# Optimization experiments

Measured on AMD Instinct MI355X. Metric: run time of the kernel, lower is better.

## Reference

```python
import jax, jax.numpy as jnp
import numpy as np

H = 256
VOCAB = 32000
B = 128
T = 2048


def setup_inputs() -> dict:
    key = jax.random.key(0)
    ks = jax.random.split(key, 14)
    s = 0.05
    return {
        "tokens": jax.random.randint(ks[0], (B, 1), 0, VOCAB),
        "hidden": jax.random.normal(ks[1], (1, B, H), jnp.float32),
        "encoder_outputs": jax.random.normal(ks[2], (T, B, H), jnp.float32),
        "emb_table": jax.random.normal(ks[3], (VOCAB + 1, H), jnp.float32) * s,
        "attn_W": jax.random.normal(ks[4], (1, 2 * H), jnp.float32) * s,
        "attn_b": jax.random.normal(ks[5], (1,), jnp.float32) * s,
        "comb_W": jax.random.normal(ks[6], (H, 2 * H), jnp.float32) * s,
        "comb_b": jax.random.normal(ks[7], (H,), jnp.float32) * s,
        "gru_Wih": jax.random.normal(ks[8], (3 * H, H), jnp.float32) * s,
        "gru_Whh": jax.random.normal(ks[9], (3 * H, H), jnp.float32) * s,
        "gru_bih": jax.random.normal(ks[10], (3 * H,), jnp.float32) * s,
        "gru_bhh": jax.random.normal(ks[11], (3 * H,), jnp.float32) * s,
        "out_W": jax.random.normal(ks[12], (VOCAB, H), jnp.float32) * s,
        "out_b": jax.random.normal(ks[13], (VOCAB,), jnp.float32) * s,
    }


def reference(tokens, hidden, encoder_outputs, emb_table, attn_W, attn_b,
              comb_W, comb_b, gru_Wih, gru_Whh, gru_bih, gru_bhh, out_W, out_b):
    h = hidden.shape[-1]
    # Embedding lookup: [B,1] -> [B,1,H] -> [1,B,H]
    emb = jnp.transpose(emb_table[tokens], (1, 0, 2))
    # Additive attention: Linear([hidden; enc_t]) -> scalar score per position.
    # attn_W splits into hidden part (first H cols) and encoder part (last H).
    W_h, W_e = attn_W[:, :h], attn_W[:, h:]          # [1,H] each
    scores = (jnp.einsum('tbh,oh->tbo', encoder_outputs, W_e)
              + jnp.einsum('lbh,oh->lbo', hidden, W_h)  # broadcast over T
              + attn_b)                                  # [T,B,1]
    attn_w = jax.nn.softmax(scores, axis=0)              # softmax over time
    # Context: weighted sum over time -> [1,B,H]
    ctx = jnp.einsum('tbo,tbh->obh', attn_w, encoder_outputs)
    # Combine embedded input with context, relu
    x = jnp.concatenate([emb, ctx], axis=2)              # [1,B,2H]
    x = jax.nn.relu(jnp.einsum('lbk,hk->lbh', x, comb_W) + comb_b)  # [1,B,H]
    # Single GRU step (PyTorch gate ordering: r, z, n)
    gx = x[0] @ gru_Wih.T + gru_bih                      # [B,3H]
    gh = hidden[0] @ gru_Whh.T + gru_bhh                 # [B,3H]
    r = jax.nn.sigmoid(gx[:, :h] + gh[:, :h])
    z = jax.nn.sigmoid(gx[:, h:2 * h] + gh[:, h:2 * h])
    n = jnp.tanh(gx[:, 2 * h:] + r * gh[:, 2 * h:])
    h_new = ((1.0 - z) * n + z * hidden[0])[None]        # [1,B,H]
    # Output projection + log_softmax over vocab
    logits = jnp.einsum('lbh,vh->lbv', h_new, out_W) + out_b
    logp = jax.nn.log_softmax(logits, axis=2)            # [1,B,V]
    return (logp, h_new, jnp.transpose(attn_w, (1, 0, 2)), ctx)
```

## Files before the change

kernel.cpp:

```cpp
#include <hip/hip_runtime.h>
#include <cstddef>

constexpr int H  = 256;
constexpr int Bb = 128;
constexpr int T  = 2048;
constexpr int V  = 32000;
constexpr int SPLITS = 16;
constexpr int TC = T / SPLITS;
constexpr int NPART = SPLITS * 4;
constexpr int NBLK = V / 64;

typedef __attribute__((ext_vector_type(8))) short short8;
typedef __attribute__((ext_vector_type(4))) float f32x4;

__device__ __forceinline__ unsigned short bf1(float a) {
  unsigned u = __builtin_bit_cast(unsigned, a);
  return (unsigned short)((u + 0x7fffu + ((u >> 16) & 1u)) >> 16);
}
__device__ __forceinline__ unsigned bfpack2(float a, float b) {
  unsigned ua = __builtin_bit_cast(unsigned, a);
  unsigned ub = __builtin_bit_cast(unsigned, b);
  ua = (ua + 0x7fffu + ((ua >> 16) & 1u)) >> 16;
  ub = (ub + 0x7fffu + ((ub >> 16) & 1u)) & 0xffff0000u;
  return ua | ub;
}

__global__ __launch_bounds__(256) void k_attn(
    const float* __restrict__ enc, const float* __restrict__ hidden,
    const float* __restrict__ attn_W, const float* __restrict__ attn_b,
    float* __restrict__ scores, float* __restrict__ ctx_part) {
  const int b = blockIdx.y, chunk = blockIdx.x;
  const int tid = threadIdx.x, lane = tid & 63, wave = tid >> 6;

  const float4 we = *(const float4*)(attn_W + H + lane * 4);
  const float4 wh = *(const float4*)(attn_W + lane * 4);
  const float4 hv = *(const float4*)(hidden + (size_t)b * H + lane * 4);

  float hb = fmaf(wh.x, hv.x, fmaf(wh.y, hv.y, fmaf(wh.z, hv.z, wh.w * hv.w)));
  #pragma unroll
  for (int off = 1; off < 64; off <<= 1) hb += __shfl_xor(hb, off);
  hb += attn_b[0];

  const int t0 = chunk * TC + wave * 32;
  const float* base = enc + (size_t)t0 * (Bb * H) + (size_t)b * H + lane * 4;

  float4 acc = {0.f, 0.f, 0.f, 0.f};
  for (int i = 0; i < 32; i += 4) {
    float4 e0 = *(const float4*)(base + (size_t)(i + 0) * (Bb * H));
    float4 e1 = *(const float4*)(base + (size_t)(i + 1) * (Bb * H));
    float4 e2 = *(const float4*)(base + (size_t)(i + 2) * (Bb * H));
    float4 e3 = *(const float4*)(base + (size_t)(i + 3) * (Bb * H));

    float p0 = fmaf(e0.x, we.x, fmaf(e0.y, we.y, fmaf(e0.z, we.z, e0.w * we.w)));
    float p1 = fmaf(e1.x, we.x, fmaf(e1.y, we.y, fmaf(e1.z, we.z, e1.w * we.w)));
    float p2 = fmaf(e2.x, we.x, fmaf(e2.y, we.y, fmaf(e2.z, we.z, e2.w * we.w)));
    float p3 = fmaf(e3.x, we.x, fmaf(e3.y, we.y, fmaf(e3.z, we.z, e3.w * we.w)));
    #pragma unroll
    for (int off = 1; off < 64; off <<= 1) {
      p0 += __shfl_xor(p0, off);
      p1 += __shfl_xor(p1, off);
      p2 += __shfl_xor(p2, off);
      p3 += __shfl_xor(p3, off);
    }
    float s0 = p0 + hb, s1 = p1 + hb, s2 = p2 + hb, s3 = p3 + hb;
    float w0 = __expf(s0), w1 = __expf(s1), w2 = __expf(s2), w3 = __expf(s3);

    acc.x = fmaf(w0, e0.x, fmaf(w1, e1.x, fmaf(w2, e2.x, fmaf(w3, e3.x, acc.x))));
    acc.y = fmaf(w0, e0.y, fmaf(w1, e1.y, fmaf(w2, e2.y, fmaf(w3, e3.y, acc.y))));
    acc.z = fmaf(w0, e0.z, fmaf(w1, e1.z, fmaf(w2, e2.z, fmaf(w3, e3.z, acc.z))));
    acc.w = fmaf(w0, e0.w, fmaf(w1, e1.w, fmaf(w2, e2.w, fmaf(w3, e3.w, acc.w))));

    if (lane == 0) {
      float4 sv = {s0, s1, s2, s3};
      *(float4*)(scores + (size_t)b * T + t0 + i) = sv;
    }
  }
  float* cp = ctx_part + ((size_t)b * NPART + chunk * 4 + wave) * H + lane * 4;
  *(float4*)cp = acc;
}

__global__ __launch_bounds__(256) void k_ctx_gru(
    const float* __restrict__ scores, const float* __restrict__ ctx_part,
    float* __restrict__ attn_o, float* __restrict__ ctx_o,
    const int* __restrict__ tokens, const float* __restrict__ hidden,
    const float* __restrict__ emb_table,
    const float* __restrict__ comb_W, const float* __restrict__ comb_b,
    const float* __restrict__ Wih, const float* __restrict__ Whh,
    const float* __restrict__ bih, const float* __restrict__ bhh,
    float* __restrict__ hnew, unsigned short* __restrict__ hnewb) {
  const int b = blockIdx.x, tid = threadIdx.x;
  const int lane = tid & 63, wave = tid >> 6;
  const int g4 = lane >> 2, l4 = lane & 3;
  __shared__ float red[4];
  __shared__ float m_sh, l_sh;
  __shared__ __align__(16) float x2[2 * H];
  __shared__ __align__(16) float hid[H];
  __shared__ __align__(16) float xs[H];
  __shared__ float Ar[H], Az[H], Cn[H], Dn[H];

  const float* sb = scores + (size_t)b * T;
  float s[8];
  #pragma unroll
  for (int q = 0; q < 8; q++) s[q] = sb[tid + 256 * q];

  float mx = s[0];
  #pragma unroll
  for (int q = 1; q < 8; q++) mx = fmaxf(mx, s[q]);
  #pragma unroll
  for (int off = 1; off < 64; off <<= 1) mx = fmaxf(mx, __shfl_xor(mx, off));
  if (lane == 0) red[wave] = mx;
  __syncthreads();
  if (tid == 0) m_sh = fmaxf(fmaxf(red[0], red[1]), fmaxf(red[2], red[3]));
  __syncthreads();
  const float m = m_sh;

  float w[8];
  float ps = 0.f;
  #pragma unroll
  for (int q = 0; q < 8; q++) { w[q] = __expf(s[q] - m); ps += w[q]; }
  #pragma unroll
  for (int off = 1; off < 64; off <<= 1) ps += __shfl_xor(ps, off);
  __syncthreads();
  if (lane == 0) red[wave] = ps;
  __syncthreads();
  if (tid == 0) l_sh = red[0] + red[1] + red[2] + red[3];
  __syncthreads();
  const float inv = 1.f / l_sh;

  #pragma unroll
  for (int q = 0; q < 8; q++) attn_o[(size_t)b * T + tid + 256 * q] = w[q] * inv;

  float c = 0.f;
  for (int si = 0; si < NPART; si++)
    c += ctx_part[((size_t)b * NPART + si) * H + tid];
  const float cval = c * __expf(-m) * inv;
  ctx_o[(size_t)b * H + tid] = cval;

  x2[tid]     = emb_table[(size_t)tokens[b] * H + tid];
  x2[H + tid] = cval;
  hid[tid]    = hidden[(size_t)b * H + tid];
  __syncthreads();

  #pragma unroll 1
  for (int batch = 0; batch < 4; batch++) {
    const int row = wave * 64 + batch * 16 + g4;
    const float* wr = comb_W + (size_t)row * (2 * H);
    float p = 0.f;
    #pragma unroll 8
    for (int i = 0; i < 32; i++) {
      const int o = i * 16 + l4 * 4;
      float4 wv = *(const float4*)(wr + o);
      float4 xv = *(const float4*)(x2 + o);
      p = fmaf(wv.x, xv.x, fmaf(wv.y, xv.y, fmaf(wv.z, xv.z, fmaf(wv.w, xv.w, p))));
    }
    p += __shfl_xor(p, 1);
    p += __shfl_xor(p, 2);
    if (l4 == 0) xs[row] = fmaxf(p + comb_b[row], 0.f);
  }
  __syncthreads();

  #pragma unroll 1
  for (int batch = 0; batch < 4; batch++) {
    const int row = wave * 64 + batch * 16 + g4;
    const float* wxr = Wih + (size_t)row * H;
    const float* wxz = Wih + (size_t)(row + H) * H;
    const float* wxn = Wih + (size_t)(row + 2 * H) * H;
    const float* whr = Whh + (size_t)row * H;
    const float* whz = Whh + (size_t)(row + H) * H;
    const float* whn = Whh + (size_t)(row + 2 * H) * H;
    float pxr = 0.f, pxz = 0.f, pxn = 0.f, phr = 0.f, phz = 0.f, phn = 0.f;
    #pragma unroll 2
    for (int i = 0; i < 16; i++) {
      const int o = i * 16 + l4 * 4;
      float4 xv = *(const float4*)(xs + o);
      float4 hv = *(const float4*)(hid + o);
      float4 a;
      a = *(const float4*)(wxr + o);
      pxr = fmaf(a.x, xv.x, fmaf(a.y, xv.y, fmaf(a.z, xv.z, fmaf(a.w, xv.w, pxr))));
      a = *(const float4*)(wxz + o);
      pxz = fmaf(a.x, xv.x, fmaf(a.y, xv.y, fmaf(a.z, xv.z, fmaf(a.w, xv.w, pxz))));
      a = *(const float4*)(wxn + o);
      pxn = fmaf(a.x, xv.x, fmaf(a.y, xv.y, fmaf(a.z, xv.z, fmaf(a.w, xv.w, pxn))));
      a = *(const float4*)(whr + o);
      phr = fmaf(a.x, hv.x, fmaf(a.y, hv.y, fmaf(a.z, hv.z, fmaf(a.w, hv.w, phr))));
      a = *(const float4*)(whz + o);
      phz = fmaf(a.x, hv.x, fmaf(a.y, hv.y, fmaf(a.z, hv.z, fmaf(a.w, hv.w, phz))));
      a = *(const float4*)(whn + o);
      phn = fmaf(a.x, hv.x, fmaf(a.y, hv.y, fmaf(a.z, hv.z, fmaf(a.w, hv.w, phn))));
    }
    float sr = pxr + phr;
    float sz = pxz + phz;
    sr  += __shfl_xor(sr, 1);  sr  += __shfl_xor(sr, 2);
    sz  += __shfl_xor(sz, 1);  sz  += __shfl_xor(sz, 2);
    pxn += __shfl_xor(pxn, 1); pxn += __shfl_xor(pxn, 2);
    phn += __shfl_xor(phn, 1); phn += __shfl_xor(phn, 2);
    if (l4 == 0) {
      Ar[row] = sr  + bih[row]         + bhh[row];
      Az[row] = sz  + bih[row + H]     + bhh[row + H];
      Cn[row] = pxn + bih[row + 2 * H];
      Dn[row] = phn + bhh[row + 2 * H];
    }
  }
  __syncthreads();

  const float rg = 1.f / (1.f + __expf(-Ar[tid]));
  const float zg = 1.f / (1.f + __expf(-Az[tid]));
  const float ng = tanhf(Cn[tid] + rg * Dn[tid]);
  const float hv = (1.f - zg) * ng + zg * hid[tid];
  hnew[(size_t)b * H + tid] = hv;
  hnewb[(size_t)b * H + tid] = bf1(hv);
}

constexpr int LSTR = 72;
__global__ __launch_bounds__(256) void k_logits(
    const unsigned short* __restrict__ hnewb, const float* __restrict__ out_W,
    const float* __restrict__ out_b, float* __restrict__ logits,
    float2* __restrict__ lse_part) {
  const int tid = threadIdx.x;
  const int lane = tid & 63, wave = tid >> 6;
  const int v0 = blockIdx.x * 64;
  const int r16 = lane & 15, quad = lane >> 4;

  __shared__ __align__(16) short lA[128 * LSTR];
  __shared__ __align__(16) short lB[64 * LSTR];
  __shared__ float2 lred[4][128];

  f32x4 acc[8];
  #pragma unroll
  for (int mt = 0; mt < 8; mt++) acc[mt] = (f32x4){0.f, 0.f, 0.f, 0.f};

  for (int k0 = 0; k0 < H; k0 += 64) {
    #pragma unroll
    for (int q = 0; q < 4; q++) {
      int idx = q * 256 + tid;
      int row = idx >> 3, c8 = idx & 7;
      f32x4 v = *(const f32x4*)(hnewb + (size_t)row * H + k0 + c8 * 8);
      *(f32x4*)(&lA[row * LSTR + c8 * 8]) = v;
    }
    #pragma unroll
    for (int q = 0; q < 4; q++) {
      int idx = q * 256 + tid;
      int row = idx >> 4, c4 = idx & 15;
      f32x4 wv = *(const f32x4*)(out_W + (size_t)(v0 + row) * H + k0 + c4 * 4);
      uint2 p;
      p.x = bfpack2(wv.x, wv.y);
      p.y = bfpack2(wv.z, wv.w);
      *(uint2*)(&lB[row * LSTR + c4 * 4]) = p;
    }
    __syncthreads();
    #pragma unroll
    for (int ks = 0; ks < 2; ks++) {
      const int brow = wave * 16 + r16;
      short8 bf = *(const short8*)(&lB[brow * LSTR + ks * 32 + quad * 8]);
      #pragma unroll
      for (int mt = 0; mt < 8; mt++) {
        short8 af = *(const short8*)(&lA[(mt * 16 + r16) * LSTR + ks * 32 + quad * 8]);
        acc[mt] = __builtin_amdgcn_mfma_f32_16x16x32_bf16(af, bf, acc[mt], 0, 0, 0);
      }
    }
    __syncthreads();
  }

  const int col0 = v0 + wave * 16 + r16;
  const float bias0 = out_b[col0];
  #pragma unroll
  for (int mt = 0; mt < 8; mt++) {
    #pragma unroll
    for (int r = 0; r < 4; r++) {
      const int brow = mt * 16 + quad * 4 + r;
      float a0 = acc[mt][r] + bias0;
      logits[(size_t)brow * V + col0] = a0;
      float mv = a0;
      #pragma unroll
      for (int off = 1; off < 16; off <<= 1) mv = fmaxf(mv, __shfl_xor(mv, off));
      float lv = __expf(a0 - mv);
      #pragma unroll
      for (int off = 1; off < 16; off <<= 1) lv += __shfl_xor(lv, off);
      if (r16 == 0) lred[wave][brow] = make_float2(mv, lv);
    }
  }
  __syncthreads();
  if (tid < 128) {
    float2 p = lred[0][tid];
    float M = p.x, L = p.y;
    #pragma unroll
    for (int w2 = 1; w2 < 4; w2++) {
      float2 q = lred[w2][tid];
      float nm = fmaxf(M, q.x);
      L = L * __expf(M - nm) + q.y * __expf(q.x - nm);
      M = nm;
    }
    lse_part[(size_t)tid * NBLK + blockIdx.x] = make_float2(M, L);
  }
}

__global__ __launch_bounds__(256) void k_sub(
    float* __restrict__ logits, const float2* __restrict__ lse_part) {
  const int b = blockIdx.y, tid = threadIdx.x;
  const int lane = tid & 63, wave = tid >> 6;

  const float2* pp = lse_part + (size_t)b * NBLK;
  float m = -1e30f, l = 0.f;
  if (tid < NBLK) { float2 p = pp[tid]; m = p.x; l = p.y; }
  if (tid + 256 < NBLK) {
    float2 p = pp[tid + 256];
    float nm = fmaxf(m, p.x);
    l = l * __expf(m - nm) + p.y * __expf(p.x - nm);
    m = nm;
  }
  #pragma unroll
  for (int off = 1; off < 64; off <<= 1) {
    float mo = __shfl_xor(m, off), lo = __shfl_xor(l, off);
    float nm = fmaxf(m, mo);
    l = l * __expf(m - nm) + lo * __expf(mo - nm);
    m = nm;
  }
  __shared__ float sm[4], sl[4];
  if (lane == 0) { sm[wave] = m; sl[wave] = l; }
  __syncthreads();
  float M = sm[0], L = sl[0];
  #pragma unroll
  for (int w2 = 1; w2 < 4; w2++) {
    float nm = fmaxf(M, sm[w2]);
    L = L * __expf(M - nm) + sl[w2] * __expf(sm[w2] - nm);
    M = nm;
  }
  const float ls = M + logf(L);

  const int i = blockIdx.x * 256 + tid;
  if (i < V / 4) {
    float4* p = (float4*)(logits + (size_t)b * V) + i;
    float4 x = *p;
    x.x -= ls; x.y -= ls; x.z -= ls; x.w -= ls;
    *p = x;
  }
}

extern "C" void kernel_launch(void* const* d_in, const int* in_sizes, int n_in,
                              void* d_out, int out_size, void* d_ws, size_t ws_size,
                              hipStream_t stream) {
  const int*   tokens = (const int*)d_in[0];
  const float* hidden = (const float*)d_in[1];
  const float* enc    = (const float*)d_in[2];
  const float* emb    = (const float*)d_in[3];
  const float* attn_W = (const float*)d_in[4];
  const float* attn_b = (const float*)d_in[5];
  const float* comb_W = (const float*)d_in[6];
  const float* comb_b = (const float*)d_in[7];
  const float* Wih    = (const float*)d_in[8];
  const float* Whh    = (const float*)d_in[9];
  const float* bih    = (const float*)d_in[10];
  const float* bhh    = (const float*)d_in[11];
  const float* out_W  = (const float*)d_in[12];
  const float* out_b  = (const float*)d_in[13];

  float* out    = (float*)d_out;
  float* logp   = out;
  float* hnew   = out + (size_t)Bb * V;
  float* attn_o = hnew + (size_t)Bb * H;
  float* ctx_o  = attn_o + (size_t)Bb * T;

  float* ws       = (float*)d_ws;
  float* scores   = ws;
  float2* lse_part = (float2*)ws;
  float* ctx_part = ws + (size_t)Bb * T;
  unsigned short* hnewb = (unsigned short*)(ctx_part + (size_t)Bb * NPART * H);

  k_attn<<<dim3(SPLITS, Bb), 256, 0, stream>>>(enc, hidden, attn_W, attn_b, scores, ctx_part);
  k_ctx_gru<<<dim3(Bb), 256, 0, stream>>>(scores, ctx_part, attn_o, ctx_o,
                                          tokens, hidden, emb, comb_W, comb_b,
                                          Wih, Whh, bih, bhh, hnew, hnewb);
  k_logits<<<dim3(V / 64), 256, 0, stream>>>(hnewb, out_W, out_b, logp, lse_part);
  k_sub<<<dim3(V / 1024 + 1, Bb), 256, 0, stream>>>(logp, lse_part);
}
```

Baseline: 493.4 us.

## Split context and GRU kernels, parallelize GRU over hidden halves, halve attention splits

Splits the fused context+GRU kernel into a context/softmax kernel that writes the concatenated input to a workspace buffer and a GRU kernel launched on a (B,2) grid, each block computing half of the hidden gates. Each GRU block still recomputes the full combine layer, so comb_W work is duplicated across the two halves. The attention kernel's time splits are halved, so each wave processes 64 timesteps and there are fewer partial contexts to reduce. The aim is more parallelism in the GRU stage and less reduction traffic, at the cost of an extra launch, a global round trip for x2, duplicated combine work and fewer attention blocks.

```diff
diff --git a/kernel.cpp b/kernel.cpp
--- a/kernel.cpp
+++ b/kernel.cpp
@@ -5,7 +5,7 @@
 constexpr int Bb = 128;
 constexpr int T  = 2048;
 constexpr int V  = 32000;
-constexpr int SPLITS = 16;
+constexpr int SPLITS = 8;
 constexpr int TC = T / SPLITS;
 constexpr int NPART = SPLITS * 4;
 constexpr int NBLK = V / 64;
@@ -41,11 +41,11 @@
   for (int off = 1; off < 64; off <<= 1) hb += __shfl_xor(hb, off);
   hb += attn_b[0];
 
-  const int t0 = chunk * TC + wave * 32;
+  const int t0 = chunk * TC + wave * 64;
   const float* base = enc + (size_t)t0 * (Bb * H) + (size_t)b * H + lane * 4;
 
   float4 acc = {0.f, 0.f, 0.f, 0.f};
-  for (int i = 0; i < 32; i += 4) {
+  for (int i = 0; i < 64; i += 4) {
     float4 e0 = *(const float4*)(base + (size_t)(i + 0) * (Bb * H));
     float4 e1 = *(const float4*)(base + (size_t)(i + 1) * (Bb * H));
     float4 e2 = *(const float4*)(base + (size_t)(i + 2) * (Bb * H));
@@ -79,24 +79,15 @@
   *(float4*)cp = acc;
 }
 
-__global__ __launch_bounds__(256) void k_ctx_gru(
+__global__ __launch_bounds__(256) void k_ctx(
     const float* __restrict__ scores, const float* __restrict__ ctx_part,
+    const int* __restrict__ tokens, const float* __restrict__ emb_table,
     float* __restrict__ attn_o, float* __restrict__ ctx_o,
-    const int* __restrict__ tokens, const float* __restrict__ hidden,
-    const float* __restrict__ emb_table,
-    const float* __restrict__ comb_W, const float* __restrict__ comb_b,
-    const float* __restrict__ Wih, const float* __restrict__ Whh,
-    const float* __restrict__ bih, const float* __restrict__ bhh,
-    float* __restrict__ hnew, unsigned short* __restrict__ hnewb) {
+    float* __restrict__ x2buf) {
   const int b = blockIdx.x, tid = threadIdx.x;
   const int lane = tid & 63, wave = tid >> 6;
-  const int g4 = lane >> 2, l4 = lane & 3;
   __shared__ float red[4];
   __shared__ float m_sh, l_sh;
-  __shared__ __align__(16) float x2[2 * H];
-  __shared__ __align__(16) float hid[H];
-  __shared__ __align__(16) float xs[H];
-  __shared__ float Ar[H], Az[H], Cn[H], Dn[H];
 
   const float* sb = scores + (size_t)b * T;
   float s[8];
@@ -136,8 +127,26 @@
   const float cval = c * __expf(-m) * inv;
   ctx_o[(size_t)b * H + tid] = cval;
 
-  x2[tid]     = emb_table[(size_t)tokens[b] * H + tid];
-  x2[H + tid] = cval;
+  x2buf[(size_t)b * (2 * H) + tid]     = emb_table[(size_t)tokens[b] * H + tid];
+  x2buf[(size_t)b * (2 * H) + H + tid] = cval;
+}
+
+__global__ __launch_bounds__(256) void k_gru(
+    const float* __restrict__ x2buf, const float* __restrict__ hidden,
+    const float* __restrict__ comb_W, const float* __restrict__ comb_b,
+    const float* __restrict__ Wih, const float* __restrict__ Whh,
+    const float* __restrict__ bih, const float* __restrict__ bhh,
+    float* __restrict__ hnew, unsigned short* __restrict__ hnewb) {
+  const int b = blockIdx.x, h = blockIdx.y, tid = threadIdx.x;
+  const int lane = tid & 63, wave = tid >> 6;
+  const int g4 = lane >> 2, l4 = lane & 3;
+  __shared__ __align__(16) float x2[2 * H];
+  __shared__ __align__(16) float hid[H];
+  __shared__ __align__(16) float xs[H];
+  __shared__ float Ar[128], Az[128], Cn[128], Dn[128];
+
+  x2[tid]     = x2buf[(size_t)b * (2 * H) + tid];
+  x2[H + tid] = x2buf[(size_t)b * (2 * H) + H + tid];
   hid[tid]    = hidden[(size_t)b * H + tid];
   __syncthreads();
 
@@ -160,8 +169,9 @@
   __syncthreads();
 
   #pragma unroll 1
-  for (int batch = 0; batch < 4; batch++) {
-    const int row = wave * 64 + batch * 16 + g4;
+  for (int batch = 0; batch < 2; batch++) {
+    const int rl  = wave * 32 + batch * 16 + g4;
+    const int row = h * 128 + rl;
     const float* wxr = Wih + (size_t)row * H;
     const float* wxz = Wih + (size_t)(row + H) * H;
     const float* wxn = Wih + (size_t)(row + 2 * H) * H;
@@ -195,20 +205,23 @@
     pxn += __shfl_xor(pxn, 1); pxn += __shfl_xor(pxn, 2);
     phn += __shfl_xor(phn, 1); phn += __shfl_xor(phn, 2);
     if (l4 == 0) {
-      Ar[row] = sr  + bih[row]         + bhh[row];
-      Az[row] = sz  + bih[row + H]     + bhh[row + H];
-      Cn[row] = pxn + bih[row + 2 * H];
-      Dn[row] = phn + bhh[row + 2 * H];
-    }
-  }
-  __syncthreads();
-
-  const float rg = 1.f / (1.f + __expf(-Ar[tid]));
-  const float zg = 1.f / (1.f + __expf(-Az[tid]));
-  const float ng = tanhf(Cn[tid] + rg * Dn[tid]);
-  const float hv = (1.f - zg) * ng + zg * hid[tid];
-  hnew[(size_t)b * H + tid] = hv;
-  hnewb[(size_t)b * H + tid] = bf1(hv);
+      Ar[rl] = sr  + bih[row]         + bhh[row];
+      Az[rl] = sz  + bih[row + H]     + bhh[row + H];
+      Cn[rl] = pxn + bih[row + 2 * H];
+      Dn[rl] = phn + bhh[row + 2 * H];
+    }
+  }
+  __syncthreads();
+
+  if (tid < 128) {
+    const int row = h * 128 + tid;
+    const float rg = 1.f / (1.f + __expf(-Ar[tid]));
+    const float zg = 1.f / (1.f + __expf(-Az[tid]));
+    const float ng = tanhf(Cn[tid] + rg * Dn[tid]);
+    const float hv = (1.f - zg) * ng + zg * hid[row];
+    hnew[(size_t)b * H + row] = hv;
+    hnewb[(size_t)b * H + row] = bf1(hv);
+  }
 }
 
 constexpr int LSTR = 72;
@@ -364,12 +377,13 @@
   float* scores   = ws;
   float2* lse_part = (float2*)ws;
   float* ctx_part = ws + (size_t)Bb * T;
-  unsigned short* hnewb = (unsigned short*)(ctx_part + (size_t)Bb * NPART * H);
+  float* x2buf    = ctx_part + (size_t)Bb * NPART * H;
+  unsigned short* hnewb = (unsigned short*)(x2buf + (size_t)Bb * 2 * H);
 
   k_attn<<<dim3(SPLITS, Bb), 256, 0, stream>>>(enc, hidden, attn_W, attn_b, scores, ctx_part);
-  k_ctx_gru<<<dim3(Bb), 256, 0, stream>>>(scores, ctx_part, attn_o, ctx_o,
-                                          tokens, hidden, emb, comb_W, comb_b,
-                                          Wih, Whh, bih, bhh, hnew, hnewb);
+  k_ctx<<<dim3(Bb), 256, 0, stream>>>(scores, ctx_part, tokens, emb, attn_o, ctx_o, x2buf);
+  k_gru<<<dim3(Bb, 2), 256, 0, stream>>>(x2buf, hidden, comb_W, comb_b,
+                                         Wih, Whh, bih, bhh, hnew, hnewb);
   k_logits<<<dim3(V / 64), 256, 0, stream>>>(hnewb, out_W, out_b, logp, lse_part);
   k_sub<<<dim3(V / 1024 + 1, Bb), 256, 0, stream>>>(logp, lse_part);
 }
```

After: 479.5 us. -2.8%, faster.
